# Optimization experiments

Measured on AMD Instinct MI355X. Metric: run time of the kernel, lower is better.

## Reference

```python
import jax, jax.numpy as jnp
import numpy as np

FP8_MAX = 448.0  # e4m3 max (use_e4m3=True)
FP8_DTYPE = jnp.float8_e4m3fn


def _quant_dequant(t):
    # scale = fp8_max / clamp(amax, 1e-12); quantize with clamp + fp8 cast; dequantize with 1/scale
    amax = jnp.maximum(jnp.abs(t).max(), 1e-12)
    scale = FP8_MAX / amax
    q = jnp.clip(t * scale, -FP8_MAX, FP8_MAX).astype(FP8_DTYPE)
    return q.astype(jnp.float32) * (1.0 / scale)


def setup_inputs() -> dict:
    key = jax.random.key(0)
    k1, k2 = jax.random.split(key)
    x = jax.random.normal(k1, (8, 2048, 4096), dtype=jnp.float32)
    weight = jax.random.normal(k2, (4096, 4096), dtype=jnp.float32) * 0.02  # (K, N)
    return {"x": x, "weight": weight}


def reference(x, weight):
    bsz, seqlen, K = x.shape
    x2d = x.reshape(-1, K)                    # (M, K)
    a32 = _quant_dequant(x2d)                 # fp8 round-trip of activations
    w32_t = _quant_dequant(weight.T)          # fp8 round-trip of transposed weight (N, K)
    out = a32 @ w32_t.T                       # (M, N) fp32 GEMM
    return out.astype(x.dtype).reshape(bsz, seqlen, -1)
```

## Files before the change

kernel.cpp:

```cpp
#include <hip/hip_runtime.h>
#include <hip/hip_bf16.h>

#define M_DIM 16384
#define N_DIM 4096
#define K_DIM 4096
#define FP8_MAX 448.0f

#define BM 256
#define BN 256
#define NK64 (K_DIM / 64)
#define NKT NK64

typedef float f32x16 __attribute__((ext_vector_type(16)));
typedef int i32x4 __attribute__((ext_vector_type(4)));
typedef int i32x8 __attribute__((ext_vector_type(8)));


__global__ void init_amax_kernel(unsigned* amax) {
    if (threadIdx.x < 2) amax[threadIdx.x] = 0u;
}

__global__ void amax_kernel(const float* __restrict__ p, long n4,
                            unsigned* __restrict__ out) {
    float m = 0.f;
    const float4* p4 = (const float4*)p;
    for (long i = (long)blockIdx.x * blockDim.x + threadIdx.x; i < n4;
         i += (long)gridDim.x * blockDim.x) {
        float4 v = p4[i];
        m = fmaxf(m, fmaxf(fmaxf(fabsf(v.x), fabsf(v.y)),
                           fmaxf(fabsf(v.z), fabsf(v.w))));
    }
#pragma unroll
    for (int off = 32; off > 0; off >>= 1)
        m = fmaxf(m, __shfl_down(m, off));
    __shared__ float smax[4];
    int lane = threadIdx.x & 63, wid = threadIdx.x >> 6;
    if (lane == 0) smax[wid] = m;
    __syncthreads();
    if (threadIdx.x == 0) {
        float bm = fmaxf(fmaxf(smax[0], smax[1]), fmaxf(smax[2], smax[3]));
        atomicMax(out, __float_as_uint(bm));
    }
}

__device__ __forceinline__ unsigned pack4(float4 v, float s) {
    float a = fminf(fmaxf(v.x * s, -FP8_MAX), FP8_MAX);
    float b = fminf(fmaxf(v.y * s, -FP8_MAX), FP8_MAX);
    float c = fminf(fmaxf(v.z * s, -FP8_MAX), FP8_MAX);
    float d = fminf(fmaxf(v.w * s, -FP8_MAX), FP8_MAX);
    int p = 0;
    p = __builtin_amdgcn_cvt_pk_fp8_f32(a, b, p, false);
    p = __builtin_amdgcn_cvt_pk_fp8_f32(c, d, p, true);
    return (unsigned)p;
}

__global__ void quant_x_kernel(const float* __restrict__ x,
                               unsigned char* __restrict__ q,
                               const unsigned* __restrict__ amax) {
    float scale = FP8_MAX / fmaxf(__uint_as_float(amax[0]), 1e-12f);
    int m32 = blockIdx.x;
    int t = threadIdx.x;
    int lane = t & 63;
    int g = t >> 6;
    int m = m32 * 32 + (lane & 31);
    int kh = lane >> 5;
    const float* rp = x + (long)m * K_DIM;
    unsigned char* ob = q + (long)m32 * NK64 * 2048;
#pragma unroll
    for (int it = 0; it < 16; ++it) {
        int k64 = it * 4 + g;
        int kb = k64 * 64 + kh * 32;
        float4 v0 = *(const float4*)&rp[kb];
        float4 v1 = *(const float4*)&rp[kb + 4];
        float4 v2 = *(const float4*)&rp[kb + 8];
        float4 v3 = *(const float4*)&rp[kb + 12];
        float4 v4 = *(const float4*)&rp[kb + 16];
        float4 v5 = *(const float4*)&rp[kb + 20];
        float4 v6 = *(const float4*)&rp[kb + 24];
        float4 v7 = *(const float4*)&rp[kb + 28];
        uint4 o0, o1;
        o0.x = pack4(v0, scale); o0.y = pack4(v1, scale);
        o0.z = pack4(v2, scale); o0.w = pack4(v3, scale);
        o1.x = pack4(v4, scale); o1.y = pack4(v5, scale);
        o1.z = pack4(v6, scale); o1.w = pack4(v7, scale);
        *(uint4*)&ob[(long)k64 * 2048 + lane * 16] = o0;
        *(uint4*)&ob[(long)k64 * 2048 + 1024 + lane * 16] = o1;
    }
}

__global__ void quant_wt_kernel(const float* __restrict__ w,
                                unsigned char* __restrict__ qw,
                                const unsigned* __restrict__ amax) {
    __shared__ unsigned tile[64][17];
    float scale = FP8_MAX / fmaxf(__uint_as_float(amax[1]), 1e-12f);
    int b = blockIdx.x;
    int bk = b & 63, bn = b >> 6;
    int k0 = bk * 64, n0 = bn * 64;
    int t = threadIdx.x;
#pragma unroll
    for (int pass = 0; pass < 4; ++pass) {
        int idx = pass * 256 + t;
        int k = idx >> 4, nw = idx & 15;
        float4 v = *(const float4*)&w[(long)(k0 + k) * N_DIM + n0 + nw * 4];
        tile[k][nw] = pack4(v, scale);
    }
    __syncthreads();
    int lane = t & 63, g = t >> 6;
    int n32 = g >> 1, h = g & 1;
    int nl = n32 * 32 + (lane & 31);
    int word = nl >> 2, sh = (nl & 3) * 8;
    int kb = (lane >> 5) * 32 + h * 16;
    uint4 o;
    unsigned* ow = (unsigned*)&o;
#pragma unroll
    for (int wd = 0; wd < 4; ++wd) {
        unsigned acc = 0;
#pragma unroll
        for (int j = 0; j < 4; ++j)
            acc |= ((tile[kb + wd * 4 + j][word] >> sh) & 0xffu) << (8 * j);
        ow[wd] = acc;
    }
    long gn32 = (long)(n0 >> 5) + n32;
    *(uint4*)&qw[(gn32 * NK64 + bk) * 2048 + h * 1024 + lane * 16] = o;
}

__device__ __forceinline__ void stage_q(const unsigned char* __restrict__ Aseg,
                                        const unsigned char* __restrict__ Bseg,
                                        unsigned char* stbuf, int tid, int kt, int r) {
    int c = r * 512 + tid;
    int f = (c >> 7) & 7;
    int q = c & 127;
    const unsigned char* src =
        ((c < 1024) ? Aseg : Bseg) + ((long)f * NK64 + kt) * 2048 + q * 16;
    __builtin_amdgcn_global_load_lds(
        (const __attribute__((address_space(1))) void*)src,
        (__attribute__((address_space(3))) void*)(stbuf + c * 16), 16, 0, 0);
}

__device__ __forceinline__ i32x8 comb(i32x4 lo, i32x4 hi) {
    return __builtin_shufflevector(lo, hi, 0, 1, 2, 3, 4, 5, 6, 7);
}

template <int VW, bool STG>
__device__ __forceinline__ void tile_step(unsigned char* sbase,
                                          const unsigned char* __restrict__ Aseg,
                                          const unsigned char* __restrict__ Bseg,
                                          int kt, int tid, int lane, int wm, int wn,
                                          f32x16 (&acc)[4][2]) {
    unsigned char* buf = sbase + (size_t)(kt & 3) * 32768;
    unsigned char* stbuf = sbase + (size_t)((kt + 3) & 3) * 32768;
    const unsigned char* Al = buf + wm * 4 * 2048;
    const unsigned char* Bl = buf + 16384 + wn * 2 * 2048;

    i32x4 a[4][2], b0lo, b0hi;
#pragma unroll
    for (int i = 0; i < 4; ++i) {
        a[i][0] = *(const i32x4*)(Al + i * 2048 + lane * 16);
        a[i][1] = *(const i32x4*)(Al + i * 2048 + 1024 + lane * 16);
    }
    b0lo = *(const i32x4*)(Bl + lane * 16);
    b0hi = *(const i32x4*)(Bl + 1024 + lane * 16);
    if (STG) {
        stage_q(Aseg, Bseg, stbuf, tid, kt + 3, 0);
        stage_q(Aseg, Bseg, stbuf, tid, kt + 3, 1);
    }
    __builtin_amdgcn_s_barrier();
    asm volatile("s_waitcnt lgkmcnt(0)" ::: "memory");
    __builtin_amdgcn_sched_barrier(0);
    __builtin_amdgcn_s_setprio(1);
    {
        i32x8 bf = comb(b0lo, b0hi);
#pragma unroll
        for (int i = 0; i < 4; ++i)
            acc[i][0] = __builtin_amdgcn_mfma_scale_f32_32x32x64_f8f6f4(
                comb(a[i][0], a[i][1]), bf, acc[i][0], 0, 0,
                0, 0x7f7f7f7f, 0, 0x7f7f7f7f);
    }
    __builtin_amdgcn_s_setprio(0);
    __builtin_amdgcn_s_barrier();

    i32x4 b1lo = *(const i32x4*)(Bl + 2048 + lane * 16);
    i32x4 b1hi = *(const i32x4*)(Bl + 2048 + 1024 + lane * 16);
    if (STG) {
        stage_q(Aseg, Bseg, stbuf, tid, kt + 3, 2);
        stage_q(Aseg, Bseg, stbuf, tid, kt + 3, 3);
    }
    __builtin_amdgcn_s_barrier();
    asm volatile("s_waitcnt lgkmcnt(0)" ::: "memory");
    __builtin_amdgcn_sched_barrier(0);
    __builtin_amdgcn_s_setprio(1);
    {
        i32x8 bf = comb(b1lo, b1hi);
#pragma unroll
        for (int i = 0; i < 4; ++i)
            acc[i][1] = __builtin_amdgcn_mfma_scale_f32_32x32x64_f8f6f4(
                comb(a[i][0], a[i][1]), bf, acc[i][1], 0, 0,
                0, 0x7f7f7f7f, 0, 0x7f7f7f7f);
    }
    __builtin_amdgcn_s_setprio(0);
    if constexpr (VW == 8) asm volatile("s_waitcnt vmcnt(8)" ::: "memory");
    else if constexpr (VW == 4) asm volatile("s_waitcnt vmcnt(4)" ::: "memory");
    else if constexpr (VW == 0) asm volatile("s_waitcnt vmcnt(0)" ::: "memory");
    if constexpr (VW >= 0) __builtin_amdgcn_s_barrier();
}

__global__ __launch_bounds__(512, 2) void gemm_fp8_kernel(
    const unsigned char* __restrict__ qa, const unsigned char* __restrict__ qw,
    float* __restrict__ out, const unsigned* __restrict__ amax) {
    __shared__ unsigned char lds[4][32768];

    int b = blockIdx.x;
    int swz = (b & 7) * 128 + (b >> 3);
    int bm = swz >> 4;
    int bn = swz & 15;

    int tid = threadIdx.x;
    int lane = tid & 63;
    int w = tid >> 6;
    int wm = w >> 2, wn = w & 3;

    f32x16 acc[4][2];
#pragma unroll
    for (int i = 0; i < 4; ++i)
#pragma unroll
        for (int j = 0; j < 2; ++j) acc[i][j] = (f32x16)0.f;

    const unsigned char* Aseg = qa + (long)(bm * 8) * NK64 * 2048;
    const unsigned char* Bseg = qw + (long)(bn * 8) * NK64 * 2048;
    unsigned char* sbase = &lds[0][0];

#pragma unroll
    for (int pt = 0; pt < 3; ++pt)
#pragma unroll
        for (int r = 0; r < 4; ++r)
            stage_q(Aseg, Bseg, sbase + (size_t)pt * 32768, tid, pt, r);
    asm volatile("s_waitcnt vmcnt(8)" ::: "memory");
    __builtin_amdgcn_s_barrier();

#pragma unroll 1
    for (int kt = 0; kt < NKT - 3; ++kt)
        tile_step<8, true>(sbase, Aseg, Bseg, kt, tid, lane, wm, wn, acc);
    tile_step<4, false>(sbase, Aseg, Bseg, NKT - 3, tid, lane, wm, wn, acc);
    tile_step<0, false>(sbase, Aseg, Bseg, NKT - 2, tid, lane, wm, wn, acc);
    tile_step<-1, false>(sbase, Aseg, Bseg, NKT - 1, tid, lane, wm, wn, acc);

    float ax = fmaxf(__uint_as_float(amax[0]), 1e-12f);
    float aw = fmaxf(__uint_as_float(amax[1]), 1e-12f);
    float s = ax * aw * (1.0f / (FP8_MAX * FP8_MAX));

    long m0 = (long)bm * BM + wm * 128;
    long n0 = (long)bn * BN + wn * 64;
    int col = lane & 31;
    int rbase = 4 * (lane >> 5);
#pragma unroll
    for (int i = 0; i < 4; ++i)
#pragma unroll
        for (int j = 0; j < 2; ++j)
#pragma unroll
            for (int reg = 0; reg < 16; ++reg) {
                int row = (reg & 3) + 8 * (reg >> 2) + rbase;
                out[(m0 + i * 32 + row) * N_DIM + n0 + j * 32 + col] =
                    acc[i][j][reg] * s;
            }
}

extern "C" void kernel_launch(void* const* d_in, const int* in_sizes, int n_in,
                              void* d_out, int out_size, void* d_ws, size_t ws_size,
                              hipStream_t stream) {
    const float* x = (const float*)d_in[0];
    const float* wgt = (const float*)d_in[1];
    float* out = (float*)d_out;

    unsigned* amax = (unsigned*)d_ws;
    unsigned char* qa = (unsigned char*)d_ws + 256;
    unsigned char* qw = qa + (long)M_DIM * K_DIM;

    init_amax_kernel<<<1, 64, 0, stream>>>(amax);
    amax_kernel<<<2048, 256, 0, stream>>>(x, (long)M_DIM * K_DIM / 4, amax + 0);
    amax_kernel<<<1024, 256, 0, stream>>>(wgt, (long)K_DIM * N_DIM / 4, amax + 1);
    quant_x_kernel<<<M_DIM / 32, 256, 0, stream>>>(x, qa, amax);
    quant_wt_kernel<<<(K_DIM / 64) * (N_DIM / 64), 256, 0, stream>>>(wgt, qw, amax);

    dim3 grid((M_DIM / BM) * (N_DIM / BN));
    gemm_fp8_kernel<<<grid, 512, 0, stream>>>(qa, qw, out, amax);
}
```

Baseline: 463.8 us.

## Double-buffer LDS fragments in registers and use one barrier per k-tile

The k-loop is rebuilt so that each step prefetches the next tile's A and B fragments from LDS into a second register set while the MFMAs consume the current set. All four global-to-LDS staging loads for tile kt+3 are issued together. This cuts synchronisation from three barriers per k-tile to one. The goal is to hide LDS read latency behind MFMA work and remove barrier stalls, at the cost of roughly 48 extra VGPRs per thread, which raises spill or occupancy risk under the 512x2 launch bound.

```diff
diff --git a/kernel.cpp b/kernel.cpp
--- a/kernel.cpp
+++ b/kernel.cpp
@@ -141,67 +141,57 @@
     return __builtin_shufflevector(lo, hi, 0, 1, 2, 3, 4, 5, 6, 7);
 }
 
-template <int VW, bool STG>
-__device__ __forceinline__ void tile_step(unsigned char* sbase,
-                                          const unsigned char* __restrict__ Aseg,
-                                          const unsigned char* __restrict__ Bseg,
-                                          int kt, int tid, int lane, int wm, int wn,
-                                          f32x16 (&acc)[4][2]) {
-    unsigned char* buf = sbase + (size_t)(kt & 3) * 32768;
-    unsigned char* stbuf = sbase + (size_t)((kt + 3) & 3) * 32768;
-    const unsigned char* Al = buf + wm * 4 * 2048;
-    const unsigned char* Bl = buf + 16384 + wn * 2 * 2048;
-
-    i32x4 a[4][2], b0lo, b0hi;
-#pragma unroll
-    for (int i = 0; i < 4; ++i) {
-        a[i][0] = *(const i32x4*)(Al + i * 2048 + lane * 16);
-        a[i][1] = *(const i32x4*)(Al + i * 2048 + 1024 + lane * 16);
-    }
-    b0lo = *(const i32x4*)(Bl + lane * 16);
-    b0hi = *(const i32x4*)(Bl + 1024 + lane * 16);
-    if (STG) {
+template <int VW, bool STG, bool NEXT>
+__device__ __forceinline__ void tile_step(
+    unsigned char* sbase, const unsigned char* __restrict__ Aseg,
+    const unsigned char* __restrict__ Bseg, int kt, int tid, int lane,
+    int wm, int wn, i32x4 (&ca)[4][2], i32x4 (&cb)[2][2],
+    i32x4 (&na)[4][2], i32x4 (&nb)[2][2], f32x16 (&acc)[4][2]) {
+    if constexpr (VW == 4)
+        asm volatile("s_waitcnt vmcnt(4) lgkmcnt(0)" ::: "memory");
+    else if constexpr (VW == 0)
+        asm volatile("s_waitcnt vmcnt(0) lgkmcnt(0)" ::: "memory");
+    if constexpr (VW >= 0) {
+        __builtin_amdgcn_sched_barrier(0);
+        __builtin_amdgcn_s_barrier();
+        __builtin_amdgcn_sched_barrier(0);
+    }
+
+    if constexpr (NEXT) {
+        const unsigned char* nbuf = sbase + (size_t)((kt + 1) & 3) * 32768;
+        const unsigned char* nAl = nbuf + wm * 4 * 2048;
+        const unsigned char* nBl = nbuf + 16384 + wn * 2 * 2048;
+#pragma unroll
+        for (int i = 0; i < 4; ++i) {
+            na[i][0] = *(const i32x4*)(nAl + i * 2048 + lane * 16);
+            na[i][1] = *(const i32x4*)(nAl + i * 2048 + 1024 + lane * 16);
+        }
+#pragma unroll
+        for (int j = 0; j < 2; ++j) {
+            nb[j][0] = *(const i32x4*)(nBl + j * 2048 + lane * 16);
+            nb[j][1] = *(const i32x4*)(nBl + j * 2048 + 1024 + lane * 16);
+        }
+    }
+    if constexpr (STG) {
+        unsigned char* stbuf = sbase + (size_t)((kt + 3) & 3) * 32768;
         stage_q(Aseg, Bseg, stbuf, tid, kt + 3, 0);
         stage_q(Aseg, Bseg, stbuf, tid, kt + 3, 1);
-    }
-    __builtin_amdgcn_s_barrier();
-    asm volatile("s_waitcnt lgkmcnt(0)" ::: "memory");
+        stage_q(Aseg, Bseg, stbuf, tid, kt + 3, 2);
+        stage_q(Aseg, Bseg, stbuf, tid, kt + 3, 3);
+    }
     __builtin_amdgcn_sched_barrier(0);
     __builtin_amdgcn_s_setprio(1);
-    {
-        i32x8 bf = comb(b0lo, b0hi);
-#pragma unroll
-        for (int i = 0; i < 4; ++i)
-            acc[i][0] = __builtin_amdgcn_mfma_scale_f32_32x32x64_f8f6f4(
-                comb(a[i][0], a[i][1]), bf, acc[i][0], 0, 0,
-                0, 0x7f7f7f7f, 0, 0x7f7f7f7f);
-    }
+#pragma unroll
+    for (int i = 0; i < 4; ++i)
+        acc[i][0] = __builtin_amdgcn_mfma_scale_f32_32x32x64_f8f6f4(
+            comb(ca[i][0], ca[i][1]), comb(cb[0][0], cb[0][1]), acc[i][0],
+            0, 0, 0, 0x7f7f7f7f, 0, 0x7f7f7f7f);
+#pragma unroll
+    for (int i = 0; i < 4; ++i)
+        acc[i][1] = __builtin_amdgcn_mfma_scale_f32_32x32x64_f8f6f4(
+            comb(ca[i][0], ca[i][1]), comb(cb[1][0], cb[1][1]), acc[i][1],
+            0, 0, 0, 0x7f7f7f7f, 0, 0x7f7f7f7f);
     __builtin_amdgcn_s_setprio(0);
-    __builtin_amdgcn_s_barrier();
-
-    i32x4 b1lo = *(const i32x4*)(Bl + 2048 + lane * 16);
-    i32x4 b1hi = *(const i32x4*)(Bl + 2048 + 1024 + lane * 16);
-    if (STG) {
-        stage_q(Aseg, Bseg, stbuf, tid, kt + 3, 2);
-        stage_q(Aseg, Bseg, stbuf, tid, kt + 3, 3);
-    }
-    __builtin_amdgcn_s_barrier();
-    asm volatile("s_waitcnt lgkmcnt(0)" ::: "memory");
-    __builtin_amdgcn_sched_barrier(0);
-    __builtin_amdgcn_s_setprio(1);
-    {
-        i32x8 bf = comb(b1lo, b1hi);
-#pragma unroll
-        for (int i = 0; i < 4; ++i)
-            acc[i][1] = __builtin_amdgcn_mfma_scale_f32_32x32x64_f8f6f4(
-                comb(a[i][0], a[i][1]), bf, acc[i][1], 0, 0,
-                0, 0x7f7f7f7f, 0, 0x7f7f7f7f);
-    }
-    __builtin_amdgcn_s_setprio(0);
-    if constexpr (VW == 8) asm volatile("s_waitcnt vmcnt(8)" ::: "memory");
-    else if constexpr (VW == 4) asm volatile("s_waitcnt vmcnt(4)" ::: "memory");
-    else if constexpr (VW == 0) asm volatile("s_waitcnt vmcnt(0)" ::: "memory");
-    if constexpr (VW >= 0) __builtin_amdgcn_s_barrier();
 }
 
 __global__ __launch_bounds__(512, 2) void gemm_fp8_kernel(
@@ -237,12 +227,37 @@
     asm volatile("s_waitcnt vmcnt(8)" ::: "memory");
     __builtin_amdgcn_s_barrier();
 
+    i32x4 A0[4][2], B0[2][2], A1[4][2], B1[2][2];
+    {
+        const unsigned char* Al = sbase + wm * 4 * 2048;
+        const unsigned char* Bl = sbase + 16384 + wn * 2 * 2048;
+#pragma unroll
+        for (int i = 0; i < 4; ++i) {
+            A0[i][0] = *(const i32x4*)(Al + i * 2048 + lane * 16);
+            A0[i][1] = *(const i32x4*)(Al + i * 2048 + 1024 + lane * 16);
+        }
+#pragma unroll
+        for (int j = 0; j < 2; ++j) {
+            B0[j][0] = *(const i32x4*)(Bl + j * 2048 + lane * 16);
+            B0[j][1] = *(const i32x4*)(Bl + j * 2048 + 1024 + lane * 16);
+        }
+    }
+
 #pragma unroll 1
-    for (int kt = 0; kt < NKT - 3; ++kt)
-        tile_step<8, true>(sbase, Aseg, Bseg, kt, tid, lane, wm, wn, acc);
-    tile_step<4, false>(sbase, Aseg, Bseg, NKT - 3, tid, lane, wm, wn, acc);
-    tile_step<0, false>(sbase, Aseg, Bseg, NKT - 2, tid, lane, wm, wn, acc);
-    tile_step<-1, false>(sbase, Aseg, Bseg, NKT - 1, tid, lane, wm, wn, acc);
+    for (int kt = 0; kt < 60; kt += 2) {
+        tile_step<4, true, true>(sbase, Aseg, Bseg, kt, tid, lane, wm, wn,
+                                 A0, B0, A1, B1, acc);
+        tile_step<4, true, true>(sbase, Aseg, Bseg, kt + 1, tid, lane, wm, wn,
+                                 A1, B1, A0, B0, acc);
+    }
+    tile_step<4, true, true>(sbase, Aseg, Bseg, 60, tid, lane, wm, wn,
+                             A0, B0, A1, B1, acc);
+    tile_step<4, false, true>(sbase, Aseg, Bseg, 61, tid, lane, wm, wn,
+                              A1, B1, A0, B0, acc);
+    tile_step<0, false, true>(sbase, Aseg, Bseg, 62, tid, lane, wm, wn,
+                              A0, B0, A1, B1, acc);
+    tile_step<-1, false, false>(sbase, Aseg, Bseg, 63, tid, lane, wm, wn,
+                                A1, B1, A0, B0, acc);
 
     float ax = fmaxf(__uint_as_float(amax[0]), 1e-12f);
     float aw = fmaxf(__uint_as_float(amax[1]), 1e-12f);
```

Measured after the change: 460.5 us. No clear change (-0.7%).
